# Optimization experiments

Measured on AMD Instinct MI355X. Metric: run time of the kernel, lower is better.

Reference implementation:

```python
import jax, jax.numpy as jnp
import numpy as np

B, N, D, D_OUT = 8, 2048, 256, 256
LN_EPS = 1e-5
LRELU_SLOPE = 0.01


def setup_inputs() -> dict:
    key = jax.random.key(0)
    ks = jax.random.split(key, 11)
    s_in = 1.0 / np.sqrt(D)
    s_out = 1.0 / np.sqrt(D)
    return {
        "x_local": jax.random.normal(ks[0], (B, N, D), dtype=jnp.float32),
        "Wq": jax.random.uniform(ks[1], (D, D), jnp.float32, -s_in, s_in),
        "bq": jax.random.uniform(ks[2], (D,), jnp.float32, -s_in, s_in),
        "Wk": jax.random.uniform(ks[3], (D, D), jnp.float32, -s_in, s_in),
        "bk": jax.random.uniform(ks[4], (D,), jnp.float32, -s_in, s_in),
        "Wv": jax.random.uniform(ks[5], (D, D), jnp.float32, -s_in, s_in),
        "bv": jax.random.uniform(ks[6], (D,), jnp.float32, -s_in, s_in),
        "Wo": jax.random.uniform(ks[7], (D_OUT, D), jnp.float32, -s_out, s_out),
        "bo": jax.random.uniform(ks[8], (D_OUT,), jnp.float32, -s_out, s_out),
        "ln_gamma": jnp.ones((D_OUT,), jnp.float32),
        "ln_beta": jnp.zeros((D_OUT,), jnp.float32),
    }


def reference(x_local, Wq, bq, Wk, bk, Wv, bv, Wo, bo, ln_gamma, ln_beta):
    # Linear layers (torch convention: y = x @ W.T + b)
    Q = jnp.einsum("bnd,ed->bne", x_local, Wq) + bq
    K = jnp.einsum("bnd,ed->bne", x_local, Wk) + bk
    V = jnp.einsum("bnd,ed->bne", x_local, Wv) + bv
    # Unscaled attention (source applies no 1/sqrt(d))
    scores = jnp.einsum("bnd,bmd->bnm", Q, K)          # [B, N, N]
    attn = jax.nn.softmax(scores, axis=-1)
    loc = jnp.einsum("bnm,bmd->bnd", attn, V)           # [B, N, D]
    # fc_out: Linear -> LayerNorm -> LeakyReLU
    h = jnp.einsum("bnd,ed->bne", loc, Wo) + bo          # [B, N, D_OUT]
    mu = jnp.mean(h, axis=-1, keepdims=True)
    var = jnp.mean(jnp.square(h - mu), axis=-1, keepdims=True)
    hn = (h - mu) / jnp.sqrt(var + LN_EPS) * ln_gamma + ln_beta
    return jnp.where(hn >= 0, hn, LRELU_SLOPE * hn)
```

## Files before the change

kernel.cpp:

```cpp
#include <hip/hip_runtime.h>

typedef unsigned short u16;
typedef __attribute__((ext_vector_type(8))) _Float16 f16x8;
typedef __attribute__((ext_vector_type(4))) float f32x4;

#define MFMA_F16 __builtin_amdgcn_mfma_f32_16x16x32_f16

static __device__ __forceinline__ u16 f2h(float f) {
    return __builtin_bit_cast(u16, (_Float16)f);
}
static __device__ __forceinline__ ushort4 f4_to_h4(const float4 v) {
    ushort4 r;
    r.x = f2h(v.x); r.y = f2h(v.y); r.z = f2h(v.z); r.w = f2h(v.w);
    return r;
}

__global__ __launch_bounds__(256) void prep_w(
    const float* __restrict__ wq, const float* __restrict__ wk,
    const float* __restrict__ wv, const float* __restrict__ wo,
    u16* __restrict__ w4)
{
    const int tid = blockIdx.x * 256 + threadIdx.x;
    for (int i = tid; i < 65536; i += 16384) {
        const float* src = (i < 16384) ? wq : (i < 32768) ? wk
                         : (i < 49152) ? wv : wo;
        ((ushort4*)w4)[i] = f4_to_h4(((const float4*)src)[i & 16383]);
    }
}

__global__ __launch_bounds__(256, 3) void proj_qkv(
    const float* __restrict__ X, const u16* __restrict__ w4,
    const float* __restrict__ bq, const float* __restrict__ bk,
    const float* __restrict__ bv,
    u16* __restrict__ Qh, u16* __restrict__ Kh, u16* __restrict__ Vt)
{
    const int z = blockIdx.y;
    const u16* __restrict__ W     = w4 + z * 65536;
    const float* __restrict__ bias = (z == 0) ? bq : (z == 1) ? bk : bv;

    const int m0   = blockIdx.x * 64;
    const int t    = threadIdx.x;
    const int w    = t >> 6;
    const int lane = t & 63;
    const int quad = lane >> 4;
    const int l16  = lane & 15;

    __shared__ __align__(16) u16 smem[18432];
    u16* Xs = smem;
    u16* Ws = smem + 2560;

    f32x4 acc[16];
#pragma unroll
    for (int i = 0; i < 16; ++i) acc[i] = f32x4{0.f, 0.f, 0.f, 0.f};

    for (int kc = 0; kc < 8; ++kc) {
#pragma unroll
        for (int i = 0; i < 2; ++i) {
            const int ch = i * 256 + t;
            const int row = ch >> 3, cg = ch & 7;
            const float4 v = *(const float4*)&X[(size_t)(m0 + row) * 256 + kc * 32 + cg * 4];
            *(ushort4*)&Xs[row * 40 + cg * 4] = f4_to_h4(v);
        }
#pragma unroll
        for (int i = 0; i < 4; ++i) {
            const int ch = i * 256 + t;
            const int row = ch >> 2, cg = ch & 3;
            *(int4*)&Ws[row * 40 + cg * 8] =
                *(const int4*)&W[(size_t)row * 256 + kc * 32 + cg * 8];
        }
        __syncthreads();

        const f16x8 af = *(const f16x8*)&Xs[(w * 16 + l16) * 40 + quad * 8];
#pragma unroll
        for (int nt = 0; nt < 16; ++nt) {
            const f16x8 bf = *(const f16x8*)&Ws[(nt * 16 + l16) * 40 + quad * 8];
            acc[nt] = MFMA_F16(af, bf, acc[nt], 0, 0, 0);
        }
        __syncthreads();
    }

    if (z < 2) {
        u16* __restrict__ Y = (z == 0) ? Qh : Kh;
#pragma unroll
        for (int nt = 0; nt < 16; ++nt) {
            const int col = nt * 16 + l16;
            const float bb = bias[col];
#pragma unroll
            for (int r = 0; r < 4; ++r)
                smem[(w * 16 + quad * 4 + r) * 264 + col] = f2h(acc[nt][r] + bb);
        }
        __syncthreads();
#pragma unroll
        for (int i = 0; i < 8; ++i) {
            const int ch = i * 256 + t;
            const int row = ch >> 5, cg = ch & 31;
            *(int4*)&Y[(size_t)(m0 + row) * 256 + cg * 8] =
                *(const int4*)&smem[row * 264 + cg * 8];
        }
    } else {
        const int b  = m0 >> 11;
        const int n0 = m0 & 2047;
#pragma unroll
        for (int nt = 0; nt < 16; ++nt) {
            const int col = nt * 16 + l16;
            const float bb = bias[col];
            ushort4 h4;
            h4.x = f2h(acc[nt][0] + bb);
            h4.y = f2h(acc[nt][1] + bb);
            h4.z = f2h(acc[nt][2] + bb);
            h4.w = f2h(acc[nt][3] + bb);
            *(ushort4*)&smem[col * 72 + w * 16 + quad * 4] = h4;
        }
        __syncthreads();
#pragma unroll
        for (int i = 0; i < 8; ++i) {
            const int ch = i * 256 + t;
            const int row = ch >> 3, cg = ch & 7;
            *(int4*)&Vt[(size_t)b * 524288 + (size_t)row * 2048 + n0 + cg * 8] =
                *(const int4*)&smem[row * 72 + cg * 8];
        }
    }
}

__global__ __launch_bounds__(256, 3) void attn(
    const u16* __restrict__ Qh, const u16* __restrict__ Kg,
    const u16* __restrict__ Vt, u16* __restrict__ Op,
    u16* __restrict__ OutS, float* __restrict__ lmpL, float* __restrict__ lmpM)
{
    const int nz = gridDim.z;
    const int z  = blockIdx.z;
    const int tbase = 64 / nz, trem = 64 % nz;
    const int my_tiles = tbase + (z < trem ? 1 : 0);
    const int tile0    = tbase * z + (z < trem ? z : trem);

    const int b  = blockIdx.y;
    const int q0 = blockIdx.x * 64;
    const int t    = threadIdx.x;
    const int w    = t >> 6;
    const int lane = t & 63;
    const int quad = lane >> 4;
    const int l16  = lane & 15;

    __shared__ __align__(16) u16 smem[18688];
    u16* Ks = smem;
    u16* Vs = smem + 8448;
    u16* Os = smem;

    f16x8 qf[8];
    {
        const size_t qrow = (size_t)(b * 2048 + q0 + w * 16 + l16) * 256;
#pragma unroll
        for (int kc = 0; kc < 8; ++kc)
            qf[kc] = *(const f16x8*)&Qh[qrow + kc * 32 + quad * 8];
    }

    f32x4 O[16];
#pragma unroll
    for (int i = 0; i < 16; ++i) O[i] = f32x4{0.f, 0.f, 0.f, 0.f};
    float mrow = -1e30f, lrow = 0.f;

    for (int it = 0; it < my_tiles; ++it) {
        const int kt = (tile0 + it) * 32;
#pragma unroll
        for (int i = 0; i < 4; ++i) {
            const int ch = i * 256 + t;
            const int row = ch >> 5, cg = ch & 31;
            const int prow = ((row >> 2) & 3) * 8 + (row >> 4) * 4 + (row & 3);
            *(int4*)&Ks[row * 264 + cg * 8] =
                *(const int4*)&Kg[(size_t)(b * 2048 + kt + prow) * 256 + cg * 8];
        }
#pragma unroll
        for (int i = 0; i < 4; ++i) {
            const int ch = i * 256 + t;
            const int row = ch >> 2, cg = ch & 3;
            *(int4*)&Vs[row * 40 + cg * 8] =
                *(const int4*)&Vt[(size_t)b * 524288 + (size_t)row * 2048 + kt + cg * 8];
        }
        __syncthreads();

        f32x4 S[2];
        S[0] = f32x4{0.f, 0.f, 0.f, 0.f};
        S[1] = f32x4{0.f, 0.f, 0.f, 0.f};
        __builtin_amdgcn_s_setprio(1);
#pragma unroll
        for (int kc = 0; kc < 8; ++kc) {
#pragma unroll
            for (int kn = 0; kn < 2; ++kn) {
                const f16x8 kf = *(const f16x8*)&Ks[(kn * 16 + l16) * 264 + kc * 32 + quad * 8];
                S[kn] = MFMA_F16(kf, qf[kc], S[kn], 0, 0, 0);
            }
        }
        __builtin_amdgcn_s_setprio(0);

        float mt = fmaxf(fmaxf(fmaxf(S[0][0], S[0][1]), fmaxf(S[0][2], S[0][3])),
                         fmaxf(fmaxf(S[1][0], S[1][1]), fmaxf(S[1][2], S[1][3])));
        mt = fmaxf(mt, __shfl_xor(mt, 16));
        mt = fmaxf(mt, __shfl_xor(mt, 32));
        if (__any(mt - mrow > 8.f)) {
            const float mnew = fmaxf(mrow, mt);
            const float a = __expf(mrow - mnew);
            lrow *= a;
#pragma unroll
            for (int dv = 0; dv < 16; ++dv)
#pragma unroll
                for (int r = 0; r < 4; ++r) O[dv][r] *= a;
            mrow = mnew;
        }
        f16x8 pfv;
        float s = 0.f;
#pragma unroll
        for (int kn = 0; kn < 2; ++kn)
#pragma unroll
            for (int r = 0; r < 4; ++r) {
                const float e = __expf(S[kn][r] - mrow);
                s += e;
                pfv[kn * 4 + r] = (_Float16)e;
            }
        s += __shfl_xor(s, 16);
        s += __shfl_xor(s, 32);
        lrow += s;

        __builtin_amdgcn_s_setprio(1);
#pragma unroll
        for (int dvt = 0; dvt < 16; ++dvt) {
            const f16x8 vf = *(const f16x8*)&Vs[(dvt * 16 + l16) * 40 + quad * 8];
            O[dvt] = MFMA_F16(vf, pfv, O[dvt], 0, 0, 0);
        }
        __builtin_amdgcn_s_setprio(0);
        __syncthreads();
    }

    {
        const float rl = 1.0f / lrow;
#pragma unroll
        for (int dvt = 0; dvt < 16; ++dvt) {
            ushort4 h4;
            h4.x = f2h(O[dvt][0] * rl);
            h4.y = f2h(O[dvt][1] * rl);
            h4.z = f2h(O[dvt][2] * rl);
            h4.w = f2h(O[dvt][3] * rl);
            *(ushort4*)&Os[(w * 16 + l16) * 264 + dvt * 16 + quad * 4] = h4;
        }
        if (quad == 0) {
            const int grow = b * 2048 + q0 + w * 16 + l16;
            lmpL[z * 16384 + grow] = lrow;
            lmpM[z * 16384 + grow] = mrow;
        }
    }
    __syncthreads();

    {
        const int row = t >> 2;
        if (z < 2) {
            u16* __restrict__ Oz = Op + (size_t)z * 4194304;
#pragma unroll
            for (int i = 0; i < 8; ++i) {
                const int chunk = (t & 3) * 8 + i;
                *(int4*)&Oz[(size_t)(b * 2048 + q0 + row) * 256 + chunk * 8] =
                    *(const int4*)&Os[row * 264 + chunk * 8];
            }
        } else {
            u16* __restrict__ Oz = OutS;
#pragma unroll
            for (int i = 0; i < 8; ++i) {
                const int chunk = (t & 3) * 8 + i;
                *(int4*)&Oz[(size_t)(b * 2048 + q0 + row) * 512 + chunk * 8] =
                    *(const int4*)&Os[row * 264 + chunk * 8];
            }
        }
    }
}

__global__ __launch_bounds__(256, 2) void outproj_ln(
    const u16* __restrict__ Op, const u16* __restrict__ OutS,
    const float* __restrict__ lmpL, const float* __restrict__ lmpM,
    const u16* __restrict__ Woh, const float* __restrict__ bo,
    const float* __restrict__ gamma, const float* __restrict__ beta,
    float* __restrict__ out)
{
    const int m0   = blockIdx.x * 32;
    const int t    = threadIdx.x;
    const int w    = t >> 6;
    const int rw   = w & 1;
    const int cw   = w >> 1;
    const int lane = t & 63;
    const int quad = lane >> 4;
    const int l16  = lane & 15;

    __shared__ __align__(16) u16 Ls[32 * 40];
    __shared__ __align__(16) u16 Ws[256 * 40];
    __shared__ _Float16 wls[3][32];
    __shared__ float part[2][16][2][2];

    if (t < 32) {
        const float l0 = lmpL[m0 + t];
        const float l1 = lmpL[16384 + m0 + t];
        const float l2 = lmpL[32768 + m0 + t];
        const float m0v = lmpM[m0 + t];
        const float m1v = lmpM[16384 + m0 + t];
        const float m2v = lmpM[32768 + m0 + t];
        const float mm = fmaxf(fmaxf(m0v, m1v), m2v);
        const float u0 = l0 * __expf(m0v - mm);
        const float u1 = l1 * __expf(m1v - mm);
        const float u2 = l2 * __expf(m2v - mm);
        const float inv = 1.0f / (u0 + u1 + u2);
        wls[0][t] = (_Float16)(u0 * inv);
        wls[1][t] = (_Float16)(u1 * inv);
        wls[2][t] = (_Float16)(u2 * inv);
    }
    __syncthreads();

    f32x4 acc[8];
#pragma unroll
    for (int i = 0; i < 8; ++i) acc[i] = f32x4{0.f, 0.f, 0.f, 0.f};

    for (int kc = 0; kc < 8; ++kc) {
        if (t < 128) {
            const int row = t >> 2, cg = t & 3;
            const size_t off  = (size_t)(m0 + row) * 256 + kc * 32 + cg * 8;
            const size_t offS = (size_t)(m0 + row) * 512 + kc * 32 + cg * 8;
            const f16x8 o0 = __builtin_bit_cast(f16x8, *(const int4*)&Op[off]);
            const f16x8 o1 = __builtin_bit_cast(f16x8, *(const int4*)&Op[4194304 + off]);
            const f16x8 o2 = __builtin_bit_cast(f16x8, *(const int4*)&OutS[offS]);
            const _Float16 w0 = wls[0][row], w1 = wls[1][row], w2 = wls[2][row];
            f16x8 lw;
#pragma unroll
            for (int j = 0; j < 8; ++j)
                lw[j] = o0[j] * w0 + o1[j] * w1 + o2[j] * w2;
            *(int4*)&Ls[row * 40 + cg * 8] = __builtin_bit_cast(int4, lw);
        }
#pragma unroll
        for (int i = 0; i < 4; ++i) {
            const int ch = i * 256 + t;
            const int row = ch >> 2, cg = ch & 3;
            *(int4*)&Ws[row * 40 + cg * 8] =
                *(const int4*)&Woh[(size_t)row * 256 + kc * 32 + cg * 8];
        }
        __syncthreads();

        const f16x8 af = *(const f16x8*)&Ls[(rw * 16 + l16) * 40 + quad * 8];
#pragma unroll
        for (int nt = 0; nt < 8; ++nt) {
            const f16x8 bf = *(const f16x8*)&Ws[((cw * 8 + nt) * 16 + l16) * 40 + quad * 8];
            acc[nt] = MFMA_F16(af, bf, acc[nt], 0, 0, 0);
        }
        __syncthreads();
    }

    float g[8], bt[8], bb[8];
#pragma unroll
    for (int nt = 0; nt < 8; ++nt) {
        const int col = cw * 128 + nt * 16 + l16;
        bb[nt] = bo[col]; g[nt] = gamma[col]; bt[nt] = beta[col];
    }

    float shv[4], sh2v[4];
#pragma unroll
    for (int r = 0; r < 4; ++r) {
        float sh = 0.f, sh2 = 0.f;
#pragma unroll
        for (int nt = 0; nt < 8; ++nt) {
            const float h = acc[nt][r] + bb[nt];
            sh  += h;
            sh2 += h * h;
        }
        sh  += __shfl_xor(sh, 1);  sh  += __shfl_xor(sh, 2);
        sh  += __shfl_xor(sh, 4);  sh  += __shfl_xor(sh, 8);
        sh2 += __shfl_xor(sh2, 1); sh2 += __shfl_xor(sh2, 2);
        sh2 += __shfl_xor(sh2, 4); sh2 += __shfl_xor(sh2, 8);
        shv[r] = sh; sh2v[r] = sh2;
    }
    if (l16 == 0) {
#pragma unroll
        for (int r = 0; r < 4; ++r) {
            part[rw][quad * 4 + r][cw][0] = shv[r];
            part[rw][quad * 4 + r][cw][1] = sh2v[r];
        }
    }
    __syncthreads();

#pragma unroll
    for (int r = 0; r < 4; ++r) {
        const float sh  = shv[r]  + part[rw][quad * 4 + r][cw ^ 1][0];
        const float sh2 = sh2v[r] + part[rw][quad * 4 + r][cw ^ 1][1];
        const float mu  = sh * (1.f / 256.f);
        const float var = fmaxf(sh2 * (1.f / 256.f) - mu * mu, 0.f);
        const float rs  = rsqrtf(var + 1e-5f);
        const size_t row = (size_t)(m0 + rw * 16 + quad * 4 + r) * 256;
#pragma unroll
        for (int nt = 0; nt < 8; ++nt) {
            const float hn = (acc[nt][r] + bb[nt] - mu) * rs * g[nt] + bt[nt];
            out[row + cw * 128 + nt * 16 + l16] = (hn >= 0.f) ? hn : 0.01f * hn;
        }
    }
}

extern "C" void kernel_launch(void* const* d_in, const int* in_sizes, int n_in,
                              void* d_out, int out_size, void* d_ws, size_t ws_size,
                              hipStream_t stream)
{
    const float* x  = (const float*)d_in[0];
    const float* Wq = (const float*)d_in[1];
    const float* bq = (const float*)d_in[2];
    const float* Wk = (const float*)d_in[3];
    const float* bk = (const float*)d_in[4];
    const float* Wv = (const float*)d_in[5];
    const float* bv = (const float*)d_in[6];
    const float* Wo = (const float*)d_in[7];
    const float* bo = (const float*)d_in[8];
    const float* gm = (const float*)d_in[9];
    const float* bt = (const float*)d_in[10];
    float* out = (float*)d_out;

    u16* W4 = (u16*)d_ws;
    u16* Qh = W4 + 262144;
    u16* Kh = Qh + 4194304;
    u16* Vt = Kh + 4194304;
    u16* Op = Vt + 4194304;
    float* lmpM = (float*)(Op + 2 * 4194304);
    float* lmpL = (float*)W4;
    u16* Woh = W4 + 196608;
    u16* OutS = (u16*)d_out;

    prep_w     <<<64,             256, 0, stream>>>(Wq, Wk, Wv, Wo, W4);
    proj_qkv   <<<dim3(256, 3),   256, 0, stream>>>(x, W4, bq, bk, bv, Qh, Kh, Vt);
    attn       <<<dim3(32, 8, 3), 256, 0, stream>>>(Qh, Kh, Vt, Op, OutS, lmpL, lmpM);
    outproj_ln <<<512,            256, 0, stream>>>(Op, OutS, lmpL, lmpM, Woh, bo, gm, bt, out);
}
```

Before: 177.4 us.

## Double-buffer K/V tiles via direct global-to-LDS loads and use two KV splits

```diff
diff --git a/kernel.cpp b/kernel.cpp
--- a/kernel.cpp
+++ b/kernel.cpp
@@ -13,6 +13,12 @@
     ushort4 r;
     r.x = f2h(v.x); r.y = f2h(v.y); r.z = f2h(v.z); r.w = f2h(v.w);
     return r;
+}
+static __device__ __forceinline__ void gl16(const u16* g, u16* l) {
+    __builtin_amdgcn_global_load_lds(
+        (__attribute__((address_space(1))) void*)(g),
+        (__attribute__((address_space(3))) void*)(l),
+        16, 0, 0);
 }
 
 __global__ __launch_bounds__(256) void prep_w(
@@ -122,16 +128,14 @@
     }
 }
 
-__global__ __launch_bounds__(256, 3) void attn(
+__global__ __launch_bounds__(256, 2) void attn(
     const u16* __restrict__ Qh, const u16* __restrict__ Kg,
-    const u16* __restrict__ Vt, u16* __restrict__ Op,
-    u16* __restrict__ OutS, float* __restrict__ lmpL, float* __restrict__ lmpM)
+    const u16* __restrict__ Vt, u16* __restrict__ Op, float* __restrict__ lmp)
 {
     const int nz = gridDim.z;
     const int z  = blockIdx.z;
-    const int tbase = 64 / nz, trem = 64 % nz;
-    const int my_tiles = tbase + (z < trem ? 1 : 0);
-    const int tile0    = tbase * z + (z < trem ? z : trem);
+    const int ntiles = 32;
+    const int tile0  = ntiles * z;
 
     const int b  = blockIdx.y;
     const int q0 = blockIdx.x * 64;
@@ -141,9 +145,7 @@
     const int quad = lane >> 4;
     const int l16  = lane & 15;
 
-    __shared__ __align__(16) u16 smem[18688];
-    u16* Ks = smem;
-    u16* Vs = smem + 8448;
+    __shared__ __align__(16) u16 smem[32768];
     u16* Os = smem;
 
     f16x8 qf[8];
@@ -154,29 +156,52 @@
             qf[kc] = *(const f16x8*)&Qh[qrow + kc * 32 + quad * 8];
     }
 
+    unsigned kgb[4], vgb[4];
+#pragma unroll
+    for (int i = 0; i < 4; ++i) {
+        const int j  = w * 4 + i;
+        const int r  = 2 * j + (lane >> 5);
+        const int pr = ((r >> 2) & 3) * 8 + (r >> 4) * 4 + (r & 3);
+        const int c  = lane & 31;
+        kgb[i] = (unsigned)((b * 2048 + pr) * 256 + ((c ^ (r & 7)) * 8));
+        const int rp = 8 * j + (lane >> 3);
+        const int c8 = lane & 7;
+        const int d  = 2 * rp + (c8 >> 2);
+        const int a  = (c8 & 3) ^ (rp & 3);
+        vgb[i] = (unsigned)(b * 524288 + d * 2048 + a * 8);
+    }
+
+#define STAGE(bufsel, kt_) do {                                              \
+        u16* Kb_ = smem + (bufsel) * 16384;                                  \
+        u16* Vb_ = Kb_ + 8192;                                               \
+        _Pragma("unroll")                                                    \
+        for (int i_ = 0; i_ < 4; ++i_) {                                     \
+            gl16(Kg + kgb[i_] + (unsigned)(kt_) * 256,                       \
+                 Kb_ + (w * 4 + i_) * 512);                                  \
+            gl16(Vt + vgb[i_] + (unsigned)(kt_),                             \
+                 Vb_ + (w * 4 + i_) * 512);                                  \
+        }                                                                    \
+    } while (0)
+
     f32x4 O[16];
 #pragma unroll
     for (int i = 0; i < 16; ++i) O[i] = f32x4{0.f, 0.f, 0.f, 0.f};
     float mrow = -1e30f, lrow = 0.f;
 
-    for (int it = 0; it < my_tiles; ++it) {
-        const int kt = (tile0 + it) * 32;
-#pragma unroll
-        for (int i = 0; i < 4; ++i) {
-            const int ch = i * 256 + t;
-            const int row = ch >> 5, cg = ch & 31;
-            const int prow = ((row >> 2) & 3) * 8 + (row >> 4) * 4 + (row & 3);
-            *(int4*)&Ks[row * 264 + cg * 8] =
-                *(const int4*)&Kg[(size_t)(b * 2048 + kt + prow) * 256 + cg * 8];
-        }
-#pragma unroll
-        for (int i = 0; i < 4; ++i) {
-            const int ch = i * 256 + t;
-            const int row = ch >> 2, cg = ch & 3;
-            *(int4*)&Vs[row * 40 + cg * 8] =
-                *(const int4*)&Vt[(size_t)b * 524288 + (size_t)row * 2048 + kt + cg * 8];
-        }
-        __syncthreads();
+    const int vbase = (l16 >> 1) * 64 + (l16 & 1) * 32
+                    + ((quad ^ ((l16 >> 1) & 3)) * 8);
+
+    STAGE(0, tile0 * 32);
+
+    for (int it = 0; it < ntiles; ++it) {
+        asm volatile("s_waitcnt vmcnt(0)" ::: "memory");
+        __builtin_amdgcn_s_barrier();
+        __builtin_amdgcn_sched_barrier(0);
+        if (it + 1 < ntiles) STAGE((it + 1) & 1, (tile0 + it + 1) * 32);
+        __builtin_amdgcn_sched_barrier(0);
+
+        const u16* Kc = smem + (it & 1) * 16384;
+        const u16* Vc = Kc + 8192;
 
         f32x4 S[2];
         S[0] = f32x4{0.f, 0.f, 0.f, 0.f};
@@ -186,7 +211,9 @@
         for (int kc = 0; kc < 8; ++kc) {
 #pragma unroll
             for (int kn = 0; kn < 2; ++kn) {
-                const f16x8 kf = *(const f16x8*)&Ks[(kn * 16 + l16) * 264 + kc * 32 + quad * 8];
+                const int r2 = kn * 16 + l16;
+                const f16x8 kf = *(const f16x8*)
+                    &Kc[r2 * 256 + (((kc * 4 + quad) ^ (l16 & 7)) * 8)];
                 S[kn] = MFMA_F16(kf, qf[kc], S[kn], 0, 0, 0);
             }
         }
@@ -223,13 +250,14 @@
         __builtin_amdgcn_s_setprio(1);
 #pragma unroll
         for (int dvt = 0; dvt < 16; ++dvt) {
-            const f16x8 vf = *(const f16x8*)&Vs[(dvt * 16 + l16) * 40 + quad * 8];
+            const f16x8 vf = *(const f16x8*)&Vc[dvt * 512 + vbase];
             O[dvt] = MFMA_F16(vf, pfv, O[dvt], 0, 0, 0);
         }
         __builtin_amdgcn_s_setprio(0);
-        __syncthreads();
-    }
-
+    }
+#undef STAGE
+
+    __syncthreads();
     {
         const float rl = 1.0f / lrow;
 #pragma unroll
@@ -243,37 +271,26 @@
         }
         if (quad == 0) {
             const int grow = b * 2048 + q0 + w * 16 + l16;
-            lmpL[z * 16384 + grow] = lrow;
-            lmpM[z * 16384 + grow] = mrow;
+            lmp[z * 16384 + grow]        = lrow;
+            lmp[(nz + z) * 16384 + grow] = mrow;
         }
     }
     __syncthreads();
 
+    u16* __restrict__ Oz = Op + (size_t)z * 4194304;
     {
         const int row = t >> 2;
-        if (z < 2) {
-            u16* __restrict__ Oz = Op + (size_t)z * 4194304;
-#pragma unroll
-            for (int i = 0; i < 8; ++i) {
-                const int chunk = (t & 3) * 8 + i;
-                *(int4*)&Oz[(size_t)(b * 2048 + q0 + row) * 256 + chunk * 8] =
-                    *(const int4*)&Os[row * 264 + chunk * 8];
-            }
-        } else {
-            u16* __restrict__ Oz = OutS;
-#pragma unroll
-            for (int i = 0; i < 8; ++i) {
-                const int chunk = (t & 3) * 8 + i;
-                *(int4*)&Oz[(size_t)(b * 2048 + q0 + row) * 512 + chunk * 8] =
-                    *(const int4*)&Os[row * 264 + chunk * 8];
-            }
+#pragma unroll
+        for (int i = 0; i < 8; ++i) {
+            const int chunk = (t & 3) * 8 + i;
+            *(int4*)&Oz[(size_t)(b * 2048 + q0 + row) * 256 + chunk * 8] =
+                *(const int4*)&Os[row * 264 + chunk * 8];
         }
     }
 }
 
 __global__ __launch_bounds__(256, 2) void outproj_ln(
-    const u16* __restrict__ Op, const u16* __restrict__ OutS,
-    const float* __restrict__ lmpL, const float* __restrict__ lmpM,
+    const u16* __restrict__ Op, const float* __restrict__ lmp,
     const u16* __restrict__ Woh, const float* __restrict__ bo,
     const float* __restrict__ gamma, const float* __restrict__ beta,
     float* __restrict__ out)
@@ -289,24 +306,18 @@
 
     __shared__ __align__(16) u16 Ls[32 * 40];
     __shared__ __align__(16) u16 Ws[256 * 40];
-    __shared__ _Float16 wls[3][32];
+    __shared__ _Float16 wls[2][32];
     __shared__ float part[2][16][2][2];
 
     if (t < 32) {
-        const float l0 = lmpL[m0 + t];
-        const float l1 = lmpL[16384 + m0 + t];
-        const float l2 = lmpL[32768 + m0 + t];
-        const float m0v = lmpM[m0 + t];
-        const float m1v = lmpM[16384 + m0 + t];
-        const float m2v = lmpM[32768 + m0 + t];
-        const float mm = fmaxf(fmaxf(m0v, m1v), m2v);
-        const float u0 = l0 * __expf(m0v - mm);
-        const float u1 = l1 * __expf(m1v - mm);
-        const float u2 = l2 * __expf(m2v - mm);
-        const float inv = 1.0f / (u0 + u1 + u2);
+        const float l0 = lmp[m0 + t],          l1 = lmp[16384 + m0 + t];
+        const float mm0 = lmp[32768 + m0 + t], mm1 = lmp[49152 + m0 + t];
+        const float mm = fmaxf(mm0, mm1);
+        const float u0 = l0 * __expf(mm0 - mm);
+        const float u1 = l1 * __expf(mm1 - mm);
+        const float inv = 1.0f / (u0 + u1);
         wls[0][t] = (_Float16)(u0 * inv);
         wls[1][t] = (_Float16)(u1 * inv);
-        wls[2][t] = (_Float16)(u2 * inv);
     }
     __syncthreads();
 
@@ -317,16 +328,13 @@
     for (int kc = 0; kc < 8; ++kc) {
         if (t < 128) {
             const int row = t >> 2, cg = t & 3;
-            const size_t off  = (size_t)(m0 + row) * 256 + kc * 32 + cg * 8;
-            const size_t offS = (size_t)(m0 + row) * 512 + kc * 32 + cg * 8;
+            const size_t off = (size_t)(m0 + row) * 256 + kc * 32 + cg * 8;
             const f16x8 o0 = __builtin_bit_cast(f16x8, *(const int4*)&Op[off]);
             const f16x8 o1 = __builtin_bit_cast(f16x8, *(const int4*)&Op[4194304 + off]);
-            const f16x8 o2 = __builtin_bit_cast(f16x8, *(const int4*)&OutS[offS]);
-            const _Float16 w0 = wls[0][row], w1 = wls[1][row], w2 = wls[2][row];
+            const _Float16 w0 = wls[0][row], w1 = wls[1][row];
             f16x8 lw;
 #pragma unroll
-            for (int j = 0; j < 8; ++j)
-                lw[j] = o0[j] * w0 + o1[j] * w1 + o2[j] * w2;
+            for (int j = 0; j < 8; ++j) lw[j] = o0[j] * w0 + o1[j] * w1;
             *(int4*)&Ls[row * 40 + cg * 8] = __builtin_bit_cast(int4, lw);
         }
 #pragma unroll
@@ -417,13 +425,11 @@
     u16* Kh = Qh + 4194304;
     u16* Vt = Kh + 4194304;
     u16* Op = Vt + 4194304;
-    float* lmpM = (float*)(Op + 2 * 4194304);
-    float* lmpL = (float*)W4;
+    float* lmp = (float*)(Op + 2 * 4194304);
     u16* Woh = W4 + 196608;
-    u16* OutS = (u16*)d_out;
 
     prep_w     <<<64,             256, 0, stream>>>(Wq, Wk, Wv, Wo, W4);
     proj_qkv   <<<dim3(256, 3),   256, 0, stream>>>(x, W4, bq, bk, bv, Qh, Kh, Vt);
-    attn       <<<dim3(32, 8, 3), 256, 0, stream>>>(Qh, Kh, Vt, Op, OutS, lmpL, lmpM);
-    outproj_ln <<<512,            256, 0, stream>>>(Op, OutS, lmpL, lmpM, Woh, bo, gm, bt, out);
-}
+    attn       <<<dim3(32, 8, 2), 256, 0, stream>>>(Qh, Kh, Vt, Op, lmp);
+    outproj_ln <<<512,            256, 0, stream>>>(Op, lmp, Woh, bo, gm, bt, out);
+}
```

Measured after the change: 170.7 us. 1.04x faster.
